# Optimization experiments

Measured on AMD Instinct MI355X. Metric: run time of the kernel, lower is better.

Reference implementation:

```python
import jax, jax.numpy as jnp
import numpy as np

OS = 14            # output_size
GRID = 2           # ceil(roi_size/OS) = ceil(28/14) = 2 (boxes are built 28x28, sampling_ratio=-1)
NODES = OS * OS    # 196 graph nodes
EPS = 1e-5         # BatchNorm eps
K, B, C, H, W = 256, 4, 256, 112, 112


def _bn_relu(x, g, b, m, v):
    # eval-mode BatchNorm2d followed by ReLU (bn_act_conv prefix)
    s = jax.lax.rsqrt(v + EPS)
    xn = (x - m[None, :, None, None]) * s[None, :, None, None]
    return jax.nn.relu(xn * g[None, :, None, None] + b[None, :, None, None])


def _conv(x, w, b, pad):
    y = jax.lax.conv_general_dilated(x, w, (1, 1), [(pad, pad), (pad, pad)],
                                     dimension_numbers=('NCHW', 'OIHW', 'NCHW'))
    return y + b[None, :, None, None]


def _roi_align(sem, boxes):
    # torchvision roi_align, spatial_scale=1.0, aligned=False, sampling_ratio=-1 (static grid=2)
    Bs, Cc, Hh, Ww = sem.shape
    bidx = boxes[:, 0].astype(jnp.int32)
    x1, y1, x2, y2 = boxes[:, 1], boxes[:, 2], boxes[:, 3], boxes[:, 4]
    bw = jnp.maximum(x2 - x1, 1.0) / OS
    bh = jnp.maximum(y2 - y1, 1.0) / OS
    t = (jnp.arange(OS * GRID, dtype=sem.dtype) + 0.5) / GRID   # pw*GRID+ix collapsed
    xs = x1[:, None] + bw[:, None] * t                          # [K, 28]
    ys = y1[:, None] + bh[:, None] * t

    def prep(c, L):
        m = (c >= -1.0) & (c <= L)
        cc = jnp.clip(c, 0.0, L - 1)
        lo = jnp.floor(cc).astype(jnp.int32)
        hi = jnp.minimum(lo + 1, L - 1)
        return m, lo, hi, cc - lo

    my, yl, yh, ly = prep(ys, Hh)
    mx, xl, xh, lx = prep(xs, Ww)
    semt = jnp.transpose(sem, (0, 2, 3, 1))  # [B,H,W,C]

    def gat(ya, xa):
        return semt[bidx[:, None, None], ya[:, :, None], xa[:, None, :]]  # [K,28,28,C]

    ly_ = ly[:, :, None, None]
    lx_ = lx[:, None, :, None]
    val = (gat(yl, xl) * (1 - ly_) * (1 - lx_) + gat(yl, xh) * (1 - ly_) * lx_
           + gat(yh, xl) * ly_ * (1 - lx_) + gat(yh, xh) * ly_ * lx_)
    val = jnp.where((my[:, :, None] & mx[:, None, :])[..., None], val, 0.0)
    val = val.reshape(-1, OS, GRID, OS, GRID, Cc).mean(axis=(2, 4))  # avg over sampling grid
    return jnp.transpose(val, (0, 3, 1, 2))  # [K,C,14,14]


def _gcn_agg(A, x):
    # PyG gcn_norm on a fully-connected weighted graph (self loops already present):
    # deg[j] = sum_i A[i,j] (scatter on col); out[j] = sum_i d^-1/2[i] A[i,j] d^-1/2[j] x[i]
    deg = A.sum(axis=1)                 # [K,196]
    dis = jax.lax.rsqrt(deg)            # sigmoid weights > 0 => no zero degree
    Nrm = dis[:, :, None] * A * dis[:, None, :]
    return jnp.einsum('kij,kif->kjf', Nrm, x)


def _forward(roi_feature, semantic, boxes,
             bn_sem_g, bn_sem_b, bn_sem_m, bn_sem_v, conv_sem_w, conv_sem_b,
             bn_fpn_g, bn_fpn_b, bn_fpn_m, bn_fpn_v, conv_fpn_w, conv_fpn_b,
             bn_aff_g, bn_aff_b, bn_aff_m, bn_aff_v, conv_aff_w, conv_aff_b,
             gcn1_w, gcn1_b, gcn2_w, gcn2_b):
    roi_sem = _roi_align(semantic, boxes)                                   # [K,256,14,14]
    a = (_conv(_bn_relu(roi_sem, bn_sem_g, bn_sem_b, bn_sem_m, bn_sem_v), conv_sem_w, conv_sem_b, 1)
         + _conv(_bn_relu(roi_feature, bn_fpn_g, bn_fpn_b, bn_fpn_m, bn_fpn_v), conv_fpn_w, conv_fpn_b, 1))
    aff = _conv(_bn_relu(a, bn_aff_g, bn_aff_b, bn_aff_m, bn_aff_v), conv_aff_w, conv_aff_b, 0)
    A = jax.nn.sigmoid(aff.reshape(-1, NODES, NODES))                       # [K,196,196]
    X = roi_feature.reshape(-1, C, NODES).transpose(0, 2, 1)                # [K,196,256] node feats
    x1 = jax.nn.relu(_gcn_agg(A, X @ gcn1_w) + gcn1_b)                      # GCNConv(256,16)+ReLU
    x2 = _gcn_agg(A, x1 @ gcn2_w) + gcn2_b                                  # GCNConv(16,256)
    emb = x2.transpose(0, 2, 1).reshape(-1, C, OS, OS)
    return roi_sem + emb


def setup_inputs() -> dict:
    key = jax.random.key(0)
    ks = jax.random.split(key, 24)
    roi_feature = jax.random.normal(ks[0], (K, C, OS, OS), jnp.float32)
    semantic = jax.random.normal(ks[1], (B, C, H, W), jnp.float32)
    bidx = jax.random.randint(ks[2], (K,), 0, B).astype(jnp.float32)
    xy = jax.random.uniform(ks[3], (K, 2), jnp.float32, 0.0, float(H - 28))
    boxes = jnp.concatenate([bidx[:, None], xy, xy + 28.0], axis=1)  # (idx,x1,y1,x2,y2), 28x28 boxes

    def bn(kg, c):
        k1, k2, k3, k4 = jax.random.split(kg, 4)
        return (jax.random.normal(k1, (c,)) * 0.1 + 1.0,
                jax.random.normal(k2, (c,)) * 0.1,
                jax.random.normal(k3, (c,)) * 0.1,
                jax.random.uniform(k4, (c,), jnp.float32, 0.5, 1.5))
    bn_sem = bn(ks[4], C); bn_fpn = bn(ks[5], C); bn_aff = bn(ks[6], 64)
    inp = {
        'roi_feature': roi_feature, 'semantic': semantic, 'boxes': boxes,
        'bn_sem_g': bn_sem[0], 'bn_sem_b': bn_sem[1], 'bn_sem_m': bn_sem[2], 'bn_sem_v': bn_sem[3],
        'conv_sem_w': jax.random.normal(ks[7], (64, C, 3, 3)) * 0.02,
        'conv_sem_b': jax.random.normal(ks[8], (64,)) * 0.02,
        'bn_fpn_g': bn_fpn[0], 'bn_fpn_b': bn_fpn[1], 'bn_fpn_m': bn_fpn[2], 'bn_fpn_v': bn_fpn[3],
        'conv_fpn_w': jax.random.normal(ks[9], (64, C, 3, 3)) * 0.02,
        'conv_fpn_b': jax.random.normal(ks[10], (64,)) * 0.02,
        'bn_aff_g': bn_aff[0], 'bn_aff_b': bn_aff[1], 'bn_aff_m': bn_aff[2], 'bn_aff_v': bn_aff[3],
        'conv_aff_w': jax.random.normal(ks[11], (NODES, 64, 1, 1)) * 0.05,
        'conv_aff_b': jax.random.normal(ks[12], (NODES,)) * 0.05,
        'gcn1_w': jax.random.normal(ks[13], (C, 16)) * 0.05,
        'gcn1_b': jax.random.normal(ks[14], (16,)) * 0.05,
        'gcn2_w': jax.random.normal(ks[15], (16, C)) * 0.05,
        'gcn2_b': jax.random.normal(ks[16], (C,)) * 0.05,
    }
    return inp


def reference(roi_feature, semantic, boxes,
              bn_sem_g, bn_sem_b, bn_sem_m, bn_sem_v, conv_sem_w, conv_sem_b,
              bn_fpn_g, bn_fpn_b, bn_fpn_m, bn_fpn_v, conv_fpn_w, conv_fpn_b,
              bn_aff_g, bn_aff_b, bn_aff_m, bn_aff_v, conv_aff_w, conv_aff_b,
              gcn1_w, gcn1_b, gcn2_w, gcn2_b):
    return _forward(roi_feature, semantic, boxes,
                    bn_sem_g, bn_sem_b, bn_sem_m, bn_sem_v, conv_sem_w, conv_sem_b,
                    bn_fpn_g, bn_fpn_b, bn_fpn_m, bn_fpn_v, conv_fpn_w, conv_fpn_b,
                    bn_aff_g, bn_aff_b, bn_aff_m, bn_aff_v, conv_aff_w, conv_aff_b,
                    gcn1_w, gcn1_b, gcn2_w, gcn2_b)
```

## Files before the change

kernel.cpp:

```cpp
#include <hip/hip_runtime.h>
#include <hip/hip_bf16.h>

#define KBOX 256
#define CCH  256
#define NODES 196
#define OS 14
#define FTQ 3211264

typedef __attribute__((ext_vector_type(8))) short  bf16x8;
typedef __attribute__((ext_vector_type(8))) unsigned short u16x8;
typedef __attribute__((ext_vector_type(4))) float  f32x4;
typedef __attribute__((ext_vector_type(4))) short  s16x4;
typedef __attribute__((ext_vector_type(4))) int    i32x4;

__device__ __forceinline__ short f2bf(float x) {
  __hip_bfloat16 h = __float2bfloat16(x);
  return *reinterpret_cast<short*>(&h);
}
__device__ __forceinline__ float bf2f(unsigned short u) {
  unsigned int x = ((unsigned int)u) << 16;
  union { unsigned int i; float f; } c; c.i = x;
  return c.f;
}

#define MFMA16 __builtin_amdgcn_mfma_f32_16x16x32_bf16

__global__ __launch_bounds__(256) void prep_kernel(
    const float* __restrict__ bn_sem_g, const float* __restrict__ bn_sem_b,
    const float* __restrict__ bn_sem_m, const float* __restrict__ bn_sem_v,
    const float* __restrict__ conv_sem_w, const float* __restrict__ conv_sem_b,
    const float* __restrict__ bn_fpn_g, const float* __restrict__ bn_fpn_b,
    const float* __restrict__ bn_fpn_m, const float* __restrict__ bn_fpn_v,
    const float* __restrict__ conv_fpn_w, const float* __restrict__ conv_fpn_b,
    const float* __restrict__ bn_aff_g, const float* __restrict__ bn_aff_b,
    const float* __restrict__ bn_aff_m, const float* __restrict__ bn_aff_v,
    const float* __restrict__ conv_aff_w, const float* __restrict__ g1w,
    const float* __restrict__ g2w,
    float* __restrict__ ss_sem, float* __restrict__ ss_fpn, float* __restrict__ ss_aff2,
    short* __restrict__ wfrag, short* __restrict__ wafrag, short* __restrict__ g1wf,
    short* __restrict__ g2wf)
{
  int gid = blockIdx.x * blockDim.x + threadIdx.x;
  int gsz = gridDim.x * blockDim.x;
  for (int c = gid; c < 256; c += gsz) {
    float s = bn_sem_g[c] * rsqrtf(bn_sem_v[c] + 1e-5f);
    ss_sem[c] = s; ss_sem[256 + c] = bn_sem_b[c] - bn_sem_m[c] * s;
    float s2 = bn_fpn_g[c] * rsqrtf(bn_fpn_v[c] + 1e-5f);
    ss_fpn[c] = s2; ss_fpn[256 + c] = bn_fpn_b[c] - bn_fpn_m[c] * s2;
  }
  for (int c = gid; c < 64; c += gsz) {
    float s = bn_aff_g[c] * rsqrtf(bn_aff_v[c] + 1e-5f);
    float sh = bn_aff_b[c] - bn_aff_m[c] * s;
    float bias = conv_sem_b[c] + conv_fpn_b[c];
    ss_aff2[c] = s; ss_aff2[64 + c] = bias * s + sh;
  }
  for (int idx = gid; idx < 144 * 4 * 64 * 8; idx += gsz) {
    int e = idx & 7, lane = (idx >> 3) & 63, nt = (idx >> 9) & 3, kstep = idx >> 11;
    int src = kstep / 72, rem = kstep % 72, icc = rem / 9, pos = rem % 9;
    int ky = pos / 3, kx = pos % 3;
    int oc = nt * 16 + (lane & 15);
    int ic = icc * 32 + (lane >> 4) * 8 + e;
    const float* w = src ? conv_fpn_w : conv_sem_w;
    wfrag[idx] = f2bf(w[((oc * 256 + ic) * 3 + ky) * 3 + kx]);
  }
  for (int idx = gid; idx < 2 * 13 * 64 * 8; idx += gsz) {
    int t = idx;
    int e = t & 7; t >>= 3;
    int lane = t & 63; t >>= 6;
    int nt = t % 13; int s = t / 13;
    int i = nt * 16 + (lane & 15);
    int ic = s * 32 + (lane >> 4) * 8 + e;
    wafrag[idx] = f2bf(i < NODES ? conv_aff_w[i * 64 + ic] : 0.f);
  }
  for (int idx = gid; idx < 8 * 64 * 8; idx += gsz) {
    int e = idx & 7, lane = (idx >> 3) & 63, ks = idx >> 9;
    int ic = ks * 32 + (lane >> 4) * 8 + e;
    int f = lane & 15;
    g1wf[idx] = f2bf(g1w[ic * 16 + f]);
  }
  for (int idx = gid; idx < 16 * 64 * 8; idx += gsz) {
    int e = idx & 7, lane = (idx >> 3) & 63, ct = idx >> 9;
    int kk = (lane >> 4) * 8 + e;
    int c = ct * 16 + (lane & 15);
    g2wf[idx] = f2bf(kk < 16 ? g2w[kk * 256 + c] : 0.f);
  }
}

__global__ __launch_bounds__(256) void transpose_bf16_kernel(
    const float* __restrict__ in, unsigned short* __restrict__ out, int C, int HW)
{
  __shared__ float tile[64][65];
  int nh = (HW + 63) >> 6;
  int bi = blockIdx.x;
  int cb = bi % (C >> 6); bi /= (C >> 6);
  int hb = bi % nh; int b = bi / nh;
  int tx = threadIdx.x & 63, ty = threadIdx.x >> 6;
  const float* inb = in + (size_t)b * C * HW;
  unsigned short* outb = out + (size_t)b * HW * C;
  #pragma unroll
  for (int i = ty; i < 64; i += 4) {
    int c = cb * 64 + i, hw = hb * 64 + tx;
    tile[i][tx] = (hw < HW) ? inb[(size_t)c * HW + hw] : 0.f;
  }
  __syncthreads();
  int cp = threadIdx.x & 31;
  #pragma unroll
  for (int i = (int)(threadIdx.x >> 5); i < 64; i += 8) {
    int hw = hb * 64 + i;
    if (hw < HW) {
      ushort2 v;
      v.x = (unsigned short)f2bf(tile[cp * 2][i]);
      v.y = (unsigned short)f2bf(tile[cp * 2 + 1][i]);
      *(ushort2*)&outb[(size_t)hw * C + cb * 64 + cp * 2] = v;
    }
  }
}

__device__ __forceinline__ void conv_one_src(
    int k, int src, int tid, char* smem,
    const unsigned short* __restrict__ roi_sem, const unsigned short* __restrict__ roif,
    const float* __restrict__ ss_sem, const float* __restrict__ ss_fpn,
    const short* __restrict__ wfrag, short* __restrict__ op_slice)
{
  short (*lds_in)[40] = (short (*)[40])smem;
  short* lds_wf = (short*)(smem + 15760);
  float* lds_sc = (float*)(smem + 52624);
  float* lds_sh = (float*)(smem + 53648);

  int wave = tid >> 6, lane = tid & 63;
  int l15 = lane & 15, lq = lane >> 4;

  {
    const float* ss = src ? ss_fpn : ss_sem;
    if (tid < 256) { lds_sc[tid] = ss[tid]; lds_sh[tid] = ss[256 + tid]; }
  }
  if (tid < 40) lds_in[196][tid] = 0;

  int mt1 = wave + 8;
  int j0 = wave * 16 + l15;
  int j1 = mt1 * 16 + l15;
  int oy0 = j0 / 14, ox0 = j0 - oy0 * 14;
  int oy1 = j1 / 14, ox1 = j1 - oy1 * 14;
  bool wave_m1 = (mt1 < 13);

  u16x8 inv2[2];
  i32x4 wv[5];
  const unsigned short* inp = (src ? roif : roi_sem) + (size_t)k * NODES * CCH;
  const short* wbase = wfrag + (size_t)src * 72 * 2048;

  f32x4 acc[2][4];
  #pragma unroll
  for (int i = 0; i < 2; ++i)
    #pragma unroll
    for (int j = 0; j < 4; ++j) acc[i][j] = f32x4{0.f, 0.f, 0.f, 0.f};

#define ISSUE_LOADS(P) do {                                                  \
    int icc_ = (P);                                                          \
    const unsigned short* in_ = inp + icc_ * 32;                             \
    inv2[0] = *(const u16x8*)(in_ + (size_t)(tid >> 2) * 256 + (tid & 3) * 8); \
    if (tid < 272) {                                                         \
      int f_ = 512 + tid;                                                    \
      inv2[1] = *(const u16x8*)(in_ + (size_t)(f_ >> 2) * 256 + (f_ & 3) * 8); \
    }                                                                        \
    const i32x4* wsl_ = (const i32x4*)(wbase + (size_t)icc_ * 9 * 2048);     \
    _Pragma("unroll")                                                        \
    for (int i_ = 0; i_ < 4; ++i_) wv[i_] = wsl_[tid + i_ * 512];            \
    if (tid < 256) wv[4] = wsl_[2048 + tid];                                 \
  } while (0)

#define WRITE_STAGE(P) do {                                                  \
    int icc_ = (P);                                                          \
    {                                                                        \
      int j_ = tid >> 2, cq_ = tid & 3;                                      \
      bf16x8 pk_;                                                            \
      _Pragma("unroll")                                                      \
      for (int u_ = 0; u_ < 8; ++u_) {                                       \
        int c_ = icc_ * 32 + cq_ * 8 + u_;                                   \
        float x_ = bf2f(inv2[0][u_]) * lds_sc[c_] + lds_sh[c_];              \
        pk_[u_] = f2bf(fmaxf(x_, 0.f));                                      \
      }                                                                      \
      *(bf16x8*)&lds_in[j_][cq_ * 8] = pk_;                                  \
    }                                                                        \
    if (tid < 272) {                                                         \
      int f_ = 512 + tid; int j_ = f_ >> 2, cq_ = f_ & 3;                    \
      bf16x8 pk_;                                                            \
      _Pragma("unroll")                                                      \
      for (int u_ = 0; u_ < 8; ++u_) {                                       \
        int c_ = icc_ * 32 + cq_ * 8 + u_;                                   \
        float x_ = bf2f(inv2[1][u_]) * lds_sc[c_] + lds_sh[c_];              \
        pk_[u_] = f2bf(fmaxf(x_, 0.f));                                      \
      }                                                                      \
      *(bf16x8*)&lds_in[j_][cq_ * 8] = pk_;                                  \
    }                                                                        \
    _Pragma("unroll")                                                        \
    for (int i_ = 0; i_ < 4; ++i_) ((i32x4*)lds_wf)[tid + i_ * 512] = wv[i_];\
    if (tid < 256) ((i32x4*)lds_wf)[2048 + tid] = wv[4];                     \
  } while (0)

  ISSUE_LOADS(0);
  __syncthreads();
  WRITE_STAGE(0);

  for (int p = 0; p < 8; ++p) {
    __syncthreads();
    if (p < 7) ISSUE_LOADS(p + 1);
    #pragma unroll
    for (int pos = 0; pos < 9; ++pos) {
      int ky = pos / 3 - 1, kx = pos % 3 - 1;
      bf16x8 bfr[4];
      #pragma unroll
      for (int n = 0; n < 4; ++n)
        bfr[n] = *(const bf16x8*)&lds_wf[((pos * 4 + n) * 64 + lane) * 8];
      {
        int ny = oy0 + ky, nx = ox0 + kx;
        bool v = ((unsigned)ny < 14u) & ((unsigned)nx < 14u);
        int np = v ? (ny * 14 + nx) : 196;
        bf16x8 afr = *(const bf16x8*)&lds_in[np][lq * 8];
        acc[0][0] = MFMA16(afr, bfr[0], acc[0][0], 0, 0, 0);
        acc[0][1] = MFMA16(afr, bfr[1], acc[0][1], 0, 0, 0);
        acc[0][2] = MFMA16(afr, bfr[2], acc[0][2], 0, 0, 0);
        acc[0][3] = MFMA16(afr, bfr[3], acc[0][3], 0, 0, 0);
      }
      if (wave_m1) {
        int ny = oy1 + ky, nx = ox1 + kx;
        bool v = (j1 < 196) & ((unsigned)ny < 14u) & ((unsigned)nx < 14u);
        int np = v ? (ny * 14 + nx) : 196;
        bf16x8 afr = *(const bf16x8*)&lds_in[np][lq * 8];
        acc[1][0] = MFMA16(afr, bfr[0], acc[1][0], 0, 0, 0);
        acc[1][1] = MFMA16(afr, bfr[1], acc[1][1], 0, 0, 0);
        acc[1][2] = MFMA16(afr, bfr[2], acc[1][2], 0, 0, 0);
        acc[1][3] = MFMA16(afr, bfr[3], acc[1][3], 0, 0, 0);
      }
    }
    __syncthreads();
    if (p < 7) WRITE_STAGE(p + 1);
  }

  #pragma unroll
  for (int mi = 0; mi < 2; ++mi) {
    int mt = wave + mi * 8;
    if (mt >= 13) continue;
    #pragma unroll
    for (int n = 0; n < 4; ++n) {
      int oc = n * 16 + l15;
      #pragma unroll
      for (int r = 0; r < 4; ++r) {
        int j = mt * 16 + lq * 4 + r;
        if (j < NODES)
          op_slice[((size_t)k * NODES + j) * 64 + oc] = f2bf(acc[mi][n][r]);
      }
    }
  }
#undef ISSUE_LOADS
#undef WRITE_STAGE
}

__global__ __launch_bounds__(512) void roi_conv1_kernel(
    const unsigned short* __restrict__ semt, const float* __restrict__ boxes,
    unsigned short* __restrict__ roi_sem,
    const unsigned short* __restrict__ roif,
    const float* __restrict__ ss_sem, const float* __restrict__ ss_fpn,
    const short* __restrict__ wfrag, short* __restrict__ a_part)
{
  __shared__ __align__(16) char smem[74240];
  int tid = threadIdx.x;
  if (blockIdx.x >= KBOX * 7) {
    int k = blockIdx.x - KBOX * 7;
    conv_one_src(k, 1, tid, smem, nullptr, roif, ss_sem, ss_fpn, wfrag, a_part + FTQ);
    return;
  }
  unsigned short (*slab)[29][256] = (unsigned short (*)[29][256])smem;
  int kb = blockIdx.x / 7, g = blockIdx.x % 7;
  int wave = tid >> 6, lane = tid & 63;
  const float* bx = boxes + kb * 5;
  int bb = (int)bx[0];
  float x1 = bx[1], y1 = bx[2];
  float xb = x1 + 0.5f, yv = y1 + 0.5f;
  int X0 = (int)floorf(xb); float fx = xb - (float)X0;
  int Y0 = (int)floorf(yv); float fy = yv - (float)Y0;
  const unsigned short* base = semt + (size_t)bb * 12544 * 256;
  #pragma unroll
  for (int i = 0; i < 19; ++i) {
    int s = wave + i * 8;
    if (s < 145) {
      int r = s / 29, xi = s - r * 29;
      int yr = min(Y0 + 4 * g + r, 111);
      int xc = min(X0 + xi, 111);
      *(s16x4*)&slab[r][xi][lane * 4] =
          *(const s16x4*)(base + ((size_t)yr * 112 + xc) * 256 + lane * 4);
    }
  }
  __syncthreads();
  int c2 = tid & 127, grp = tid >> 7;
  int oyl = grp >> 1, og = grp & 1;
  int rb = oyl * 2;
  float w0 = 1.f - fy;
  unsigned short* op = roi_sem + (((size_t)kb * NODES) + (2 * g + oyl) * OS) * 256 + c2 * 2;
  #pragma unroll
  for (int oxs = 0; oxs < 7; ++oxs) {
    int ox = og * 7 + oxs;
    float o0 = 0.f, o1 = 0.f;
    #pragma unroll
    for (int xi = 0; xi < 3; ++xi) {
      float xw = (xi == 0) ? (1.f - fx) : (xi == 1 ? 1.f : fx);
      const unsigned short* p0 = &slab[rb][2 * ox + xi][c2 * 2];
      const unsigned short* p1 = &slab[rb + 1][2 * ox + xi][c2 * 2];
      const unsigned short* p2 = &slab[rb + 2][2 * ox + xi][c2 * 2];
      o0 += xw * (w0 * bf2f(p0[0]) + bf2f(p1[0]) + fy * bf2f(p2[0]));
      o1 += xw * (w0 * bf2f(p0[1]) + bf2f(p1[1]) + fy * bf2f(p2[1]));
    }
    ushort2 v;
    v.x = (unsigned short)f2bf(o0 * 0.25f);
    v.y = (unsigned short)f2bf(o1 * 0.25f);
    *(ushort2*)(op + (size_t)ox * 256) = v;
  }
}

__global__ __launch_bounds__(512) void conv0_kernel(
    const unsigned short* __restrict__ roi_sem, const unsigned short* __restrict__ roif,
    const float* __restrict__ ss_sem, const float* __restrict__ ss_fpn,
    const short* __restrict__ wfrag, short* __restrict__ a_part)
{
  __shared__ __align__(16) char smem[54672];
  conv_one_src(blockIdx.x, 0, threadIdx.x, smem, roi_sem, roif, ss_sem, ss_fpn,
               wfrag, a_part);
}

__global__ __launch_bounds__(1024, 1) void graph_kernel(
    const short* __restrict__ a_part, const float* __restrict__ ss_aff2,
    const short* __restrict__ wafrag,
    const float* __restrict__ aff_b, const short* __restrict__ g1wf,
    const float* __restrict__ g1b, const unsigned short* __restrict__ roif_bf,
    const short* __restrict__ g2wf, const float* __restrict__ g2b,
    const unsigned short* __restrict__ roi_sem, float* __restrict__ outp)
{
  __shared__ __align__(16) char smem[125840];
  const int tid = threadIdx.x, wave = tid >> 6, lane = tid & 63;
  const int l15 = lane & 15, lq = lane >> 4;
  const int k = blockIdx.x;

  char*  Ab   = smem;
  short* wa   = (short*)(smem + 96512);
  short* yfr  = (short*)(smem + 96512);
  short* zsf  = (short*)(smem + 103680);
  float* dsl  = (float*)(smem + 123136);
  float* g1bl = (float*)(smem + 123968);
  float* g2bl = (float*)(smem + 124032);
  float* affb = (float*)(smem + 125056);

  const bool wv13 = (wave < 13);
  const int jr  = wave * 16 + l15;
  const int jrc = min(jr, 195);
  const i32x4 z4 = {};
  const unsigned short* rsmk = roi_sem + (size_t)k * 50176;

  bf16x8 af0 = {}, af1 = {};
  if (wv13) {
    float s0[8] = {0,0,0,0,0,0,0,0}, s1[8] = {0,0,0,0,0,0,0,0};
    #pragma unroll
    for (int sl = 0; sl < 2; ++sl) {
      const unsigned short* p = (const unsigned short*)a_part + (size_t)sl * FTQ
                                + ((size_t)k * NODES + jrc) * 64 + lq * 8;
      u16x8 v0 = *(const u16x8*)p;
      u16x8 v1 = *(const u16x8*)(p + 32);
      #pragma unroll
      for (int e = 0; e < 8; ++e) { s0[e] += bf2f(v0[e]); s1[e] += bf2f(v1[e]); }
    }
    #pragma unroll
    for (int e = 0; e < 8; ++e) {
      int oc0 = lq * 8 + e, oc1 = 32 + lq * 8 + e;
      af0[e] = f2bf(fmaxf(s0[e] * ss_aff2[oc0] + ss_aff2[64 + oc0], 0.f));
      af1[e] = f2bf(fmaxf(s1[e] * ss_aff2[oc1] + ss_aff2[64 + oc1], 0.f));
    }
  }
  {
    i32x4 w0 = ((const i32x4*)wafrag)[tid];
    i32x4 w1 = z4;
    if (tid < 640) w1 = ((const i32x4*)wafrag)[1024 + tid];
    if (tid < 832) {
      int r = tid >> 2, q = tid & 3;
      *(i32x4*)(Ab + r * 464 + 384 + q * 16) = z4;
    }
    if (tid < 196) affb[tid] = aff_b[tid];
    if (tid < 256) g2bl[tid] = g2b[tid];
    if (tid < 16)  g1bl[tid] = g1b[tid];
    ((i32x4*)wa)[tid] = w0;
    if (tid < 640) ((i32x4*)wa)[1024 + tid] = w1;
  }
  __syncthreads();

  if (wv13) {
    float rsum[4] = {0.f, 0.f, 0.f, 0.f};
    #pragma unroll
    for (int n = 0; n < 13; ++n) {
      bf16x8 b0 = *(const bf16x8*)(wa + (n * 64 + lane) * 8);
      bf16x8 b1 = *(const bf16x8*)(wa + ((13 + n) * 64 + lane) * 8);
      f32x4 acc = {0.f, 0.f, 0.f, 0.f};
      acc = MFMA16(af0, b0, acc, 0, 0, 0);
      acc = MFMA16(af1, b1, acc, 0, 0, 0);
      int i = n * 16 + l15;
      bool iv = (i < 196);
      float bv = affb[iv ? i : 0];
      #pragma unroll
      for (int r = 0; r < 4; ++r) {
        float v = acc[r] + bv;
        float s = 1.f / (1.f + __expf(-v));
        if (iv) {
          rsum[r] += s;
          *(short*)(Ab + (wave * 16 + lq * 4 + r) * 464 + i * 2) = f2bf(s);
        }
      }
    }
    #pragma unroll
    for (int r = 0; r < 4; ++r) {
      float v = rsum[r];
      v += __shfl_xor(v, 1); v += __shfl_xor(v, 2);
      v += __shfl_xor(v, 4); v += __shfl_xor(v, 8);
      int j = wave * 16 + lq * 4 + r;
      if (l15 == 0 && j < 196) dsl[j] = rsqrtf(v);
    }
  }
  __syncthreads();

  *(i32x4*)(smem + 96512 + tid * 16) = z4;
  if (tid < 256) *(i32x4*)(smem + 96512 + (1024 + tid) * 16) = z4;
  f32x4 xacc = {0.f, 0.f, 0.f, 0.f};
  if (wv13) {
    const unsigned short* Xp = roif_bf + (size_t)k * 50176 + (size_t)jrc * 256 + lq * 8;
    #pragma unroll
    for (int ks = 0; ks < 8; ++ks) {
      bf16x8 xa = *(const bf16x8*)(Xp + ks * 32);
      bf16x8 xb = *(const bf16x8*)(g1wf + (ks * 64 + lane) * 8);
      xacc = MFMA16(xa, xb, xacc, 0, 0, 0);
    }
  }
  __syncthreads();

  if (wv13) {
    #pragma unroll
    for (int r = 0; r < 4; ++r) {
      int i = wave * 16 + lq * 4 + r;
      if (i < 196) {
        float yv = dsl[i] * xacc[r];
        yfr[((i >> 5) * 64 + ((i >> 3) & 3) * 16 + l15) * 8 + (i & 7)] = f2bf(yv);
      }
    }
  }
  __syncthreads();

  f32x4 g0 = {0.f, 0.f, 0.f, 0.f};
  if (wv13) {
    #pragma unroll
    for (int ks = 0; ks < 7; ++ks) {
      bf16x8 bb = *(const bf16x8*)(yfr + (ks * 64 + lane) * 8);
      bf16x8 a0 = *(const bf16x8*)(Ab + jr * 464 + ks * 64 + lq * 16);
      g0 = MFMA16(a0, bb, g0, 0, 0, 0);
    }
  }
  __syncthreads();
  if (wv13) {
    #pragma unroll
    for (int r = 0; r < 4; ++r) {
      int i = wave * 16 + lq * 4 + r;
      if (i < 196) {
        float d = dsl[i];
        float x1v = fmaxf(g0[r] * d + g1bl[l15], 0.f);
        yfr[((i >> 5) * 64 + ((i >> 3) & 3) * 16 + l15) * 8 + (i & 7)] = f2bf(d * x1v);
      }
    }
  }
  __syncthreads();

  u16x8 pre0[3];
  #pragma unroll
  for (int it = 0; it < 3; ++it) {
    int v = tid + it * 1024;
    int row = v >> 5, cq = v & 31;
    pre0[it] = *(const u16x8*)(rsmk + (size_t)row * 256 + cq * 8);
  }

  if (wv13) {
    f32x4 z0 = {0.f, 0.f, 0.f, 0.f};
    #pragma unroll
    for (int ks = 0; ks < 7; ++ks) {
      bf16x8 bb = *(const bf16x8*)(yfr + (ks * 64 + lane) * 8);
      bf16x8 a0 = *(const bf16x8*)(Ab + jr * 464 + ks * 64 + lq * 16);
      z0 = MFMA16(a0, bb, z0, 0, 0, 0);
    }
    #pragma unroll
    for (int r = 0; r < 4; ++r) {
      int j = wave * 16 + lq * 4 + r;
      if (j < 196) {
        float zv = z0[r] * dsl[j];
        zsf[((j >> 4) * 64 + (l15 >> 3) * 16 + (j & 15)) * 8 + (l15 & 7)] = f2bf(zv);
      }
    }
  }
  __syncthreads();

  {
    bf16x8 wf = *(const bf16x8*)(g2wf + (wave * 64 + lane) * 8);
    float* op = outp + (size_t)k * 50176;
    unsigned short* rst = (unsigned short*)smem;
    const int c_ = wave * 16 + lq * 4;
    float gbv[4];
    #pragma unroll
    for (int r = 0; r < 4; ++r) gbv[r] = g2bl[c_ + r];
    #pragma unroll
    for (int it = 0; it < 3; ++it) {
      int v = tid + it * 1024;
      int row = v >> 5, cq = v & 31;
      *(u16x8*)&rst[row * 264 + cq * 8] = pre0[it];
    }
    __syncthreads();
    u16x8 pre1[4];
    #pragma unroll
    for (int it = 0; it < 4; ++it) {
      int v = tid + it * 1024;
      if (v < 3200) {
        int row = v >> 5, cq = v & 31;
        pre1[it] = *(const u16x8*)(rsmk + (size_t)(96 + row) * 256 + cq * 8);
      }
    }
    #pragma unroll
    for (int jt = 0; jt < 6; ++jt) {
      bf16x8 zb = *(const bf16x8*)(zsf + (jt * 64 + lane) * 8);
      f32x4 d = {0.f, 0.f, 0.f, 0.f};
      d = MFMA16(wf, zb, d, 0, 0, 0);
      int j = jt * 16 + l15;
      const unsigned short* rr = rst + j * 264 + c_;
      unsigned int p01 = *(const unsigned int*)rr;
      unsigned int p23 = *(const unsigned int*)(rr + 2);
      op[(size_t)(c_ + 0) * 196 + j] = d[0] + gbv[0] + bf2f((unsigned short)(p01 & 0xffff));
      op[(size_t)(c_ + 1) * 196 + j] = d[1] + gbv[1] + bf2f((unsigned short)(p01 >> 16));
      op[(size_t)(c_ + 2) * 196 + j] = d[2] + gbv[2] + bf2f((unsigned short)(p23 & 0xffff));
      op[(size_t)(c_ + 3) * 196 + j] = d[3] + gbv[3] + bf2f((unsigned short)(p23 >> 16));
    }
    __syncthreads();
    #pragma unroll
    for (int it = 0; it < 4; ++it) {
      int v = tid + it * 1024;
      if (v < 3200) {
        int row = v >> 5, cq = v & 31;
        *(u16x8*)&rst[row * 264 + cq * 8] = pre1[it];
      }
    }
    __syncthreads();
    #pragma unroll
    for (int jt = 6; jt < 13; ++jt) {
      bf16x8 zb = *(const bf16x8*)(zsf + (jt * 64 + lane) * 8);
      f32x4 d = {0.f, 0.f, 0.f, 0.f};
      d = MFMA16(wf, zb, d, 0, 0, 0);
      int j = jt * 16 + l15;
      if (j < 196) {
        const unsigned short* rr = rst + (j - 96) * 264 + c_;
        unsigned int p01 = *(const unsigned int*)rr;
        unsigned int p23 = *(const unsigned int*)(rr + 2);
        op[(size_t)(c_ + 0) * 196 + j] = d[0] + gbv[0] + bf2f((unsigned short)(p01 & 0xffff));
        op[(size_t)(c_ + 1) * 196 + j] = d[1] + gbv[1] + bf2f((unsigned short)(p01 >> 16));
        op[(size_t)(c_ + 2) * 196 + j] = d[2] + gbv[2] + bf2f((unsigned short)(p23 & 0xffff));
        op[(size_t)(c_ + 3) * 196 + j] = d[3] + gbv[3] + bf2f((unsigned short)(p23 >> 16));
      }
    }
  }
}

extern "C" void kernel_launch(void* const* d_in, const int* in_sizes, int n_in,
                              void* d_out, int out_size, void* d_ws, size_t ws_size,
                              hipStream_t stream) {
  const float* roi_feature = (const float*)d_in[0];
  const float* semantic    = (const float*)d_in[1];
  const float* boxes       = (const float*)d_in[2];
  const float* bn_sem_g = (const float*)d_in[3];
  const float* bn_sem_b = (const float*)d_in[4];
  const float* bn_sem_m = (const float*)d_in[5];
  const float* bn_sem_v = (const float*)d_in[6];
  const float* conv_sem_w = (const float*)d_in[7];
  const float* conv_sem_b = (const float*)d_in[8];
  const float* bn_fpn_g = (const float*)d_in[9];
  const float* bn_fpn_b = (const float*)d_in[10];
  const float* bn_fpn_m = (const float*)d_in[11];
  const float* bn_fpn_v = (const float*)d_in[12];
  const float* conv_fpn_w = (const float*)d_in[13];
  const float* conv_fpn_b = (const float*)d_in[14];
  const float* bn_aff_g = (const float*)d_in[15];
  const float* bn_aff_b = (const float*)d_in[16];
  const float* bn_aff_m = (const float*)d_in[17];
  const float* bn_aff_v = (const float*)d_in[18];
  const float* conv_aff_w = (const float*)d_in[19];
  const float* conv_aff_b = (const float*)d_in[20];
  const float* gcn1_w = (const float*)d_in[21];
  const float* gcn1_b = (const float*)d_in[22];
  const float* gcn2_w = (const float*)d_in[23];
  const float* gcn2_b = (const float*)d_in[24];

  const size_t FT = (size_t)KBOX * NODES * CCH;
  unsigned short* ws16      = (unsigned short*)d_ws;
  unsigned short* semt_bf   = ws16;
  unsigned short* roif_bf   = semt_bf + FT;
  unsigned short* roi_sem_b = roif_bf + FT;
  short*          a_part    = (short*)(roi_sem_b + FT);
  float*          ss_sem    = (float*)(a_part + 2 * (size_t)FTQ);
  float*          ss_fpn    = ss_sem + 512;
  float*          ss_aff2   = ss_fpn + 512;
  short*          wfrag     = (short*)(ss_aff2 + 128);
  short*          wafrag    = wfrag + 294912;
  short*          g1wf      = wafrag + 13312;
  short*          g2wf      = g1wf + 4096;

  prep_kernel<<<256, 256, 0, stream>>>(
      bn_sem_g, bn_sem_b, bn_sem_m, bn_sem_v, conv_sem_w, conv_sem_b,
      bn_fpn_g, bn_fpn_b, bn_fpn_m, bn_fpn_v, conv_fpn_w, conv_fpn_b,
      bn_aff_g, bn_aff_b, bn_aff_m, bn_aff_v, conv_aff_w, gcn1_w, gcn2_w,
      ss_sem, ss_fpn, ss_aff2, wfrag, wafrag, g1wf, g2wf);

  transpose_bf16_kernel<<<4 * 4 * 256, 256, 0, stream>>>(roi_feature, roif_bf, 256, 196);
  transpose_bf16_kernel<<<4 * 196 * 4, 256, 0, stream>>>(semantic, semt_bf, 256, 12544);
  roi_conv1_kernel<<<KBOX * 7 + KBOX, 512, 0, stream>>>(
      semt_bf, boxes, roi_sem_b, roif_bf, ss_sem, ss_fpn, wfrag, a_part);
  conv0_kernel<<<KBOX, 512, 0, stream>>>(roi_sem_b, roif_bf, ss_sem, ss_fpn, wfrag, a_part);
  graph_kernel<<<KBOX, 1024, 0, stream>>>(a_part, ss_aff2, wafrag, conv_aff_b, g1wf, gcn1_b,
                                          roif_bf, g2wf, gcn2_b, roi_sem_b, (float*)d_out);
}
```

Baseline: 148.1 us.

## Split conv0 input channels across two blocks and interleave fpn conv blocks

```diff
diff --git a/kernel.cpp b/kernel.cpp
--- a/kernel.cpp
+++ b/kernel.cpp
@@ -117,7 +117,7 @@
 }
 
 __device__ __forceinline__ void conv_one_src(
-    int k, int src, int tid, char* smem,
+    int k, int src, int icc0, int np, int tid, char* smem,
     const unsigned short* __restrict__ roi_sem, const unsigned short* __restrict__ roif,
     const float* __restrict__ ss_sem, const float* __restrict__ ss_fpn,
     const short* __restrict__ wfrag, short* __restrict__ op_slice)
@@ -155,7 +155,7 @@
     for (int j = 0; j < 4; ++j) acc[i][j] = f32x4{0.f, 0.f, 0.f, 0.f};
 
 #define ISSUE_LOADS(P) do {                                                  \
-    int icc_ = (P);                                                          \
+    int icc_ = icc0 + (P);                                                   \
     const unsigned short* in_ = inp + icc_ * 32;                             \
     inv2[0] = *(const u16x8*)(in_ + (size_t)(tid >> 2) * 256 + (tid & 3) * 8); \
     if (tid < 272) {                                                         \
@@ -169,7 +169,7 @@
   } while (0)
 
 #define WRITE_STAGE(P) do {                                                  \
-    int icc_ = (P);                                                          \
+    int icc_ = icc0 + (P);                                                   \
     {                                                                        \
       int j_ = tid >> 2, cq_ = tid & 3;                                      \
       bf16x8 pk_;                                                            \
@@ -201,9 +201,9 @@
   __syncthreads();
   WRITE_STAGE(0);
 
-  for (int p = 0; p < 8; ++p) {
+  for (int p = 0; p < np; ++p) {
     __syncthreads();
-    if (p < 7) ISSUE_LOADS(p + 1);
+    if (p < np - 1) ISSUE_LOADS(p + 1);
     #pragma unroll
     for (int pos = 0; pos < 9; ++pos) {
       int ky = pos / 3 - 1, kx = pos % 3 - 1;
@@ -214,8 +214,8 @@
       {
         int ny = oy0 + ky, nx = ox0 + kx;
         bool v = ((unsigned)ny < 14u) & ((unsigned)nx < 14u);
-        int np = v ? (ny * 14 + nx) : 196;
-        bf16x8 afr = *(const bf16x8*)&lds_in[np][lq * 8];
+        int np_ = v ? (ny * 14 + nx) : 196;
+        bf16x8 afr = *(const bf16x8*)&lds_in[np_][lq * 8];
         acc[0][0] = MFMA16(afr, bfr[0], acc[0][0], 0, 0, 0);
         acc[0][1] = MFMA16(afr, bfr[1], acc[0][1], 0, 0, 0);
         acc[0][2] = MFMA16(afr, bfr[2], acc[0][2], 0, 0, 0);
@@ -224,8 +224,8 @@
       if (wave_m1) {
         int ny = oy1 + ky, nx = ox1 + kx;
         bool v = (j1 < 196) & ((unsigned)ny < 14u) & ((unsigned)nx < 14u);
-        int np = v ? (ny * 14 + nx) : 196;
-        bf16x8 afr = *(const bf16x8*)&lds_in[np][lq * 8];
+        int np_ = v ? (ny * 14 + nx) : 196;
+        bf16x8 afr = *(const bf16x8*)&lds_in[np_][lq * 8];
         acc[1][0] = MFMA16(afr, bfr[0], acc[1][0], 0, 0, 0);
         acc[1][1] = MFMA16(afr, bfr[1], acc[1][1], 0, 0, 0);
         acc[1][2] = MFMA16(afr, bfr[2], acc[1][2], 0, 0, 0);
@@ -233,7 +233,7 @@
       }
     }
     __syncthreads();
-    if (p < 7) WRITE_STAGE(p + 1);
+    if (p < np - 1) WRITE_STAGE(p + 1);
   }
 
   #pragma unroll
@@ -264,13 +264,13 @@
 {
   __shared__ __align__(16) char smem[74240];
   int tid = threadIdx.x;
-  if (blockIdx.x >= KBOX * 7) {
-    int k = blockIdx.x - KBOX * 7;
-    conv_one_src(k, 1, tid, smem, nullptr, roif, ss_sem, ss_fpn, wfrag, a_part + FTQ);
+  int kb = blockIdx.x >> 3, r7 = blockIdx.x & 7;
+  if (r7 == 7) {
+    conv_one_src(kb, 1, 0, 8, tid, smem, nullptr, roif, ss_sem, ss_fpn, wfrag, a_part);
     return;
   }
   unsigned short (*slab)[29][256] = (unsigned short (*)[29][256])smem;
-  int kb = blockIdx.x / 7, g = blockIdx.x % 7;
+  int g = r7;
   int wave = tid >> 6, lane = tid & 63;
   const float* bx = boxes + kb * 5;
   int bb = (int)bx[0];
@@ -283,10 +283,10 @@
   for (int i = 0; i < 19; ++i) {
     int s = wave + i * 8;
     if (s < 145) {
-      int r = s / 29, xi = s - r * 29;
-      int yr = min(Y0 + 4 * g + r, 111);
+      int rr = s / 29, xi = s - rr * 29;
+      int yr = min(Y0 + 4 * g + rr, 111);
       int xc = min(X0 + xi, 111);
-      *(s16x4*)&slab[r][xi][lane * 4] =
+      *(s16x4*)&slab[rr][xi][lane * 4] =
           *(const s16x4*)(base + ((size_t)yr * 112 + xc) * 256 + lane * 4);
     }
   }
@@ -322,8 +322,9 @@
     const short* __restrict__ wfrag, short* __restrict__ a_part)
 {
   __shared__ __align__(16) char smem[54672];
-  conv_one_src(blockIdx.x, 0, threadIdx.x, smem, roi_sem, roif, ss_sem, ss_fpn,
-               wfrag, a_part);
+  int k = blockIdx.x >> 1, ih = blockIdx.x & 1;
+  conv_one_src(k, 0, ih * 4, 4, threadIdx.x, smem, roi_sem, roif, ss_sem, ss_fpn,
+               wfrag, a_part + (size_t)(1 + ih) * FTQ);
 }
 
 __global__ __launch_bounds__(1024, 1) void graph_kernel(
@@ -358,7 +359,7 @@
   if (wv13) {
     float s0[8] = {0,0,0,0,0,0,0,0}, s1[8] = {0,0,0,0,0,0,0,0};
     #pragma unroll
-    for (int sl = 0; sl < 2; ++sl) {
+    for (int sl = 0; sl < 3; ++sl) {
       const unsigned short* p = (const unsigned short*)a_part + (size_t)sl * FTQ
                                 + ((size_t)k * NODES + jrc) * 64 + lq * 8;
       u16x8 v0 = *(const u16x8*)p;
@@ -600,7 +601,7 @@
   unsigned short* roif_bf   = semt_bf + FT;
   unsigned short* roi_sem_b = roif_bf + FT;
   short*          a_part    = (short*)(roi_sem_b + FT);
-  float*          ss_sem    = (float*)(a_part + 2 * (size_t)FTQ);
+  float*          ss_sem    = (float*)(a_part + 3 * (size_t)FTQ);
   float*          ss_fpn    = ss_sem + 512;
   float*          ss_aff2   = ss_fpn + 512;
   short*          wfrag     = (short*)(ss_aff2 + 128);
@@ -616,9 +617,9 @@
 
   transpose_bf16_kernel<<<4 * 4 * 256, 256, 0, stream>>>(roi_feature, roif_bf, 256, 196);
   transpose_bf16_kernel<<<4 * 196 * 4, 256, 0, stream>>>(semantic, semt_bf, 256, 12544);
-  roi_conv1_kernel<<<KBOX * 7 + KBOX, 512, 0, stream>>>(
+  roi_conv1_kernel<<<KBOX * 8, 512, 0, stream>>>(
       semt_bf, boxes, roi_sem_b, roif_bf, ss_sem, ss_fpn, wfrag, a_part);
-  conv0_kernel<<<KBOX, 512, 0, stream>>>(roi_sem_b, roif_bf, ss_sem, ss_fpn, wfrag, a_part);
+  conv0_kernel<<<KBOX * 2, 512, 0, stream>>>(roi_sem_b, roif_bf, ss_sem, ss_fpn, wfrag, a_part);
   graph_kernel<<<KBOX, 1024, 0, stream>>>(a_part, ss_aff2, wafrag, conv_aff_b, g1wf, gcn1_b,
                                           roif_bf, g2wf, gcn2_b, roi_sem_b, (float*)d_out);
 }
```

After: 259.9 us. 75.5% more time.
